# Optimization experiments

Measured on AMD Instinct MI355X. Metric: run time of the kernel, lower is better.

## Reference

```python
import jax, jax.numpy as jnp
import numpy as np

NA = 3            # anchors per scale
NC = 80           # num classes
THRESH = 0.6      # wh-IoU anchor-match threshold
EPS = 1e-7

ANCHORS_PX = np.array([[12,16],[19,36],[40,28],[36,75],[76,55],[72,146],
                       [142,110],[192,243],[459,401]], dtype=np.float32).reshape(3, 3, 2)


def setup_inputs() -> dict:
    key = jax.random.key(0)
    k1, k2, k3, k4, k5, k6 = jax.random.split(key, 6)
    B, M = 16, 32
    p0 = jax.random.normal(k1, (B, NA * (5 + NC), 80, 80), jnp.float32)
    p1 = jax.random.normal(k2, (B, NA * (5 + NC), 40, 40), jnp.float32)
    p2 = jax.random.normal(k3, (B, NA * (5 + NC), 20, 20), jnp.float32)
    # targets: [B, M, 6] = (img_idx, class in [1,NC], cx, cy, w, h) normalized to [0,1]
    bidx = jnp.broadcast_to(jnp.arange(B, dtype=jnp.float32)[:, None], (B, M))
    cls = jax.random.randint(k4, (B, M), 1, NC + 1).astype(jnp.float32)
    xy = jax.random.uniform(k5, (B, M, 2), minval=0.05, maxval=0.95)
    ka, kj = jax.random.split(k6)
    aidx = jax.random.randint(ka, (B, M), 0, 9)
    base_wh = jnp.asarray(ANCHORS_PX.reshape(9, 2))[aidx] / 640.0
    jitter = jnp.exp(jax.random.uniform(kj, (B, M, 2), minval=-0.15, maxval=0.15))
    wh = base_wh * jitter
    targets = jnp.concatenate([bidx[..., None], cls[..., None], xy, wh], axis=-1)
    return {"p0": p0, "p1": p1, "p2": p2,
            "targets": targets,
            "anchors": jnp.asarray(ANCHORS_PX),
            "image_size": jnp.array([640.0, 640.0], jnp.float32)}


def _bce_logits(x, t):
    # BCEWithLogits, pos_weight=1, elementwise
    return jnp.maximum(x, 0.0) - x * t + jnp.log1p(jnp.exp(-jnp.abs(x)))


def _giou(pbox, tbox):
    # boxes [N,4] in cxcywh
    px1 = pbox[:, 0] - pbox[:, 2] * 0.5
    py1 = pbox[:, 1] - pbox[:, 3] * 0.5
    px2 = pbox[:, 0] + pbox[:, 2] * 0.5
    py2 = pbox[:, 1] + pbox[:, 3] * 0.5
    tx1 = tbox[:, 0] - tbox[:, 2] * 0.5
    ty1 = tbox[:, 1] - tbox[:, 3] * 0.5
    tx2 = tbox[:, 0] + tbox[:, 2] * 0.5
    ty2 = tbox[:, 1] + tbox[:, 3] * 0.5
    iw = jnp.clip(jnp.minimum(px2, tx2) - jnp.maximum(px1, tx1), 0.0)
    ih = jnp.clip(jnp.minimum(py2, ty2) - jnp.maximum(py1, ty1), 0.0)
    inter = iw * ih
    union = pbox[:, 2] * pbox[:, 3] + tbox[:, 2] * tbox[:, 3] - inter + EPS
    iou = inter / union
    cw = jnp.maximum(px2, tx2) - jnp.minimum(px1, tx1)
    ch = jnp.maximum(py2, ty2) - jnp.minimum(py1, ty1)
    c_area = cw * ch + EPS
    return iou - (c_area - union) / c_area


def _scale_losses(pi, tflat, anchors_i, image_size):
    # pi: [B, NA*(5+NC), H, W]; tflat: [N,6]; anchors_i: [NA,2] in pixels
    B = pi.shape[0]
    H, W = pi.shape[-2:]
    stride = image_size / jnp.array([H, W], jnp.float32)          # (sH, sW)
    anchor = anchors_i / stride[::-1][None, :]                    # anchors in grid units (w,h)
    gain = jnp.concatenate([jnp.ones((2,), jnp.float32),
                            (1.0 / stride)[jnp.array([1, 0, 1, 0])]])
    t = tflat * gain                                              # [N,6]
    gwh = t[:, 4:6]
    # wh-IoU matrix [NA, N] -> best anchor per target
    inter = (jnp.minimum(anchor[:, None, 0], gwh[None, :, 0])
             * jnp.minimum(anchor[:, None, 1], gwh[None, :, 1]))
    union = anchor[:, None, 0] * anchor[:, None, 1] + gwh[None, :, 0] * gwh[None, :, 1] - inter
    iou = inter / union
    best = iou.max(0)
    a = iou.argmax(0)
    mask = best > THRESH                                          # fixed-shape mask replaces torch boolean compaction
    maskf = mask.astype(jnp.float32)

    b = jnp.where(mask, t[:, 0].astype(jnp.int32), 0)
    c = t[:, 1].astype(jnp.int32)
    gxy = t[:, 2:4]
    gi = jnp.where(mask, gxy[:, 0].astype(jnp.int32), 0)
    gj = jnp.where(mask, gxy[:, 1].astype(jnp.int32), 0)
    a_s = jnp.where(mask, a, 0)

    pir = pi.reshape(B, NA, 5 + NC, H, W).transpose(0, 1, 3, 4, 2)  # [B,NA,H,W,5+NC]
    ps = pir[b, a_s, gj, gi]                                        # [N,5+NC]
    tobj = jnp.zeros((B, NA, H, W), jnp.float32)
    tobj = tobj.at[b, a_s, gj, gi].max(jax.lax.stop_gradient(maskf))

    pxy = jax.nn.sigmoid(ps[:, 0:2])
    pwh = jnp.minimum(jnp.exp(ps[:, 2:4]), 1000.0) * anchor[a_s]
    pbox = jnp.concatenate([pxy, pwh], 1)
    tbox = jnp.concatenate([gxy % 1.0, t[:, 4:6]], 1)
    giou = _giou(pbox, tbox)
    nb = jnp.maximum(maskf.sum(), 1.0)
    lbox = (maskf * (1.0 - giou)).sum() / nb
    tcls = jax.nn.one_hot(c - 1, NC, dtype=jnp.float32)             # cp=1, cn=0 (eps=0)
    lcls = (maskf[:, None] * _bce_logits(ps[:, 5:], tcls)).sum() / (nb * NC)
    lobj = _bce_logits(pir[..., 4], tobj).mean()
    return lbox, lobj, lcls


def _total_loss(p0, p1, p2, targets, anchors, image_size):
    tflat = targets.reshape(-1, 6)
    lbox = lobj = lcls = jnp.float32(0.0)
    for i, pi in enumerate([p0, p1, p2]):
        lb, lo, lc = _scale_losses(pi, tflat, anchors[i], image_size)
        lbox = lbox + lb
        lobj = lobj + lo
        lcls = lcls + lc
    lbox = lbox * 3.54
    lobj = lobj * 64.3
    lcls = lcls * 37.4
    return lbox + lobj + lcls, lbox, lobj, lcls


def reference(p0, p1, p2, targets, anchors, image_size):
    return _total_loss(p0, p1, p2, targets, anchors, image_size)
```

## Files before the change

kernel.cpp:

```cpp
#include <hip/hip_runtime.h>
#include <math.h>

#define NAANCH 3
#define NCLS 80
#define BATCH 16
#define NTGT 512
#define CH 85

#define V4_S0 76800
#define V4_S1 19200
#define V4_S2 4800
#define V4_TOT (V4_S0 + V4_S1 + V4_S2)
#define OBJ_BLOCKS 197
#define GRID_BLOCKS (3 + OBJ_BLOCKS)

#define WBOX 3.54f
#define WOBJ 64.3f
#define WCLS 37.4f

__device__ __forceinline__ float bce0(float x) {
    return fmaxf(x, 0.0f) + log1pf(expf(-fabsf(x)));
}

__device__ __forceinline__ float wave_sum(float v) {
    for (int off = 32; off > 0; off >>= 1) v += __shfl_down(v, off, 64);
    return v;
}

__global__ void yolo_loss_kernel(const float* __restrict__ p0,
                                 const float* __restrict__ p1,
                                 const float* __restrict__ p2,
                                 const float* __restrict__ targets,
                                 const float* __restrict__ anchors,
                                 const float* __restrict__ image_size,
                                 float* __restrict__ out) {
    const int tid  = threadIdx.x;
    const int lane = tid & 63;
    const int wid  = tid >> 6;

    __shared__ int   sh_key[NTGT];
    __shared__ int   sh_off[NTGT];
    __shared__ int   sh_ci[NTGT];
    __shared__ unsigned char sh_mk[NTGT];
    __shared__ float red[4][8];

    if (blockIdx.x < 3) {
        const int s = blockIdx.x;
        const int j = tid;
        const int H = (s == 0) ? 80 : ((s == 1) ? 40 : 20);
        const int W = H;
        const int HW = H * W;
        const float* pi = (s == 0) ? p0 : ((s == 1) ? p1 : p2);

        const float stride0 = image_size[0] / (float)H;
        const float stride1 = image_size[1] / (float)W;
        const float gx = 1.0f / stride1;
        const float gy = 1.0f / stride0;

        const float t0 = targets[j * 6 + 0];
        const float t1 = targets[j * 6 + 1];
        const float tx = targets[j * 6 + 2] * gx;
        const float ty = targets[j * 6 + 3] * gy;
        const float gw = targets[j * 6 + 4] * gx;
        const float gh = targets[j * 6 + 5] * gy;

        float best = -1.0f; int abest = 0;
        for (int k = 0; k < NAANCH; ++k) {
            float aw = anchors[(s * NAANCH + k) * 2 + 0] / stride1;
            float ah = anchors[(s * NAANCH + k) * 2 + 1] / stride0;
            float inter = fminf(aw, gw) * fminf(ah, gh);
            float uni = aw * ah + gw * gh - inter;
            float iou = inter / uni;
            if (iou > best) { best = iou; abest = k; }
        }
        const bool  mask  = best > 0.6f;
        const float maskf = mask ? 1.0f : 0.0f;

        int b  = mask ? (int)t0 : 0;
        const int c = (int)t1;
        int gi = mask ? (int)tx : 0;
        int gj = mask ? (int)ty : 0;
        const int a_s = mask ? abest : 0;
        gi = min(max(gi, 0), W - 1);
        gj = min(max(gj, 0), H - 1);
        b  = min(max(b, 0), BATCH - 1);

        const int key = ((b * NAANCH + a_s) * H + gj) * W + gi;
        const int off = (b * (NAANCH * CH) + a_s * CH) * HW + gj * W + gi;

        float lbox_t = 0.0f, ps4 = 0.0f;
        if (mask) {
            const float ps0 = pi[off + 0 * HW];
            const float ps1 = pi[off + 1 * HW];
            const float ps2 = pi[off + 2 * HW];
            const float ps3 = pi[off + 3 * HW];
            ps4 = pi[off + 4 * HW];

            const float aw = anchors[(s * NAANCH + a_s) * 2 + 0] / stride1;
            const float ah = anchors[(s * NAANCH + a_s) * 2 + 1] / stride0;

            const float pxc = 1.0f / (1.0f + expf(-ps0));
            const float pyc = 1.0f / (1.0f + expf(-ps1));
            const float pw  = fminf(expf(ps2), 1000.0f) * aw;
            const float ph  = fminf(expf(ps3), 1000.0f) * ah;
            const float txc = tx - floorf(tx);
            const float tyc = ty - floorf(ty);

            const float px1 = pxc - pw * 0.5f, py1 = pyc - ph * 0.5f;
            const float px2 = pxc + pw * 0.5f, py2 = pyc + ph * 0.5f;
            const float qx1 = txc - gw * 0.5f, qy1 = tyc - gh * 0.5f;
            const float qx2 = txc + gw * 0.5f, qy2 = tyc + gh * 0.5f;
            const float iw = fmaxf(fminf(px2, qx2) - fmaxf(px1, qx1), 0.0f);
            const float ih = fmaxf(fminf(py2, qy2) - fmaxf(py1, qy1), 0.0f);
            const float inter = iw * ih;
            const float uni = pw * ph + gw * gh - inter + 1e-7f;
            const float iou = inter / uni;
            const float cw  = fmaxf(px2, qx2) - fminf(px1, qx1);
            const float chh = fmaxf(py2, qy2) - fminf(py1, qy1);
            const float carea = cw * chh + 1e-7f;
            lbox_t = 1.0f - (iou - (carea - uni) / carea);
        }

        sh_key[j] = key;
        sh_off[j] = off;
        sh_ci[j]  = c - 1;
        sh_mk[j]  = mask ? 1 : 0;
        __syncthreads();

        float corr = 0.0f;
        if (mask) {
            bool dup = false;
            for (int j2 = 0; j2 < j; ++j2)
                if (sh_mk[j2] && sh_key[j2] == key) { dup = true; break; }
            if (!dup) corr = -ps4;
        }

        float v0 = wave_sum(lbox_t);
        float v1 = wave_sum(maskf);
        float v2 = wave_sum(corr);
        if (lane == 0) { red[0][wid] = v0; red[1][wid] = v1; red[2][wid] = v2; }
        __syncthreads();

        float lcls_w = 0.0f;
        for (int j2 = wid; j2 < NTGT; j2 += 8) {
            if (!sh_mk[j2]) continue;
            const int toff = sh_off[j2];
            const int ci   = sh_ci[j2];
            const int k1 = lane;
            float x1 = pi[toff + (5 + k1) * HW];
            float c1 = bce0(x1) - ((k1 == ci) ? x1 : 0.0f);
            float c2 = 0.0f;
            if (lane < NCLS - 64) {
                const int k2 = 64 + lane;
                float x2 = pi[toff + (5 + k2) * HW];
                c2 = bce0(x2) - ((k2 == ci) ? x2 : 0.0f);
            }
            float tsum = wave_sum(c1 + c2);
            if (lane == 0) lcls_w += tsum;
        }
        if (lane == 0) red[3][wid] = lcls_w;
        __syncthreads();

        if (tid == 0) {
            float acc[4] = {0.f, 0.f, 0.f, 0.f};
            for (int w = 0; w < 8; ++w) {
                acc[0] += red[0][w]; acc[1] += red[1][w];
                acc[2] += red[2][w]; acc[3] += red[3][w];
            }
            const float Ns = (s == 0) ? 307200.0f : ((s == 1) ? 76800.0f : 19200.0f);
            const float nb = fmaxf(acc[1], 1.0f);
            const float lbox_c = WBOX * (acc[0] / nb);
            const float lobj_c = WOBJ * (acc[2] / Ns);
            const float lcls_c = WCLS * (acc[3] / (nb * (float)NCLS));
            atomicAdd(&out[1], lbox_c);
            atomicAdd(&out[2], lobj_c);
            atomicAdd(&out[3], lcls_c);
            atomicAdd(&out[0], lbox_c + lobj_c + lcls_c);
        }
    } else {
        const int vb = (blockIdx.x - 3) * 512 + tid;
        float a0 = 0.f, a1 = 0.f, a2 = 0.f;
        if (vb < V4_TOT) {
            const float4* addr; int hw4; int sflag;
            if (vb < V4_S0) {
                const int u = vb;
                const int ba = u / 1600;  hw4 = u - ba * 1600;
                const int b = ba / 3, a = ba - 3 * b;
                addr = (const float4*)(p0 + (size_t)((b * NAANCH + a) * CH + 4) * 6400);
                sflag = 0;
            } else if (vb < V4_S0 + V4_S1) {
                const int u = vb - V4_S0;
                const int ba = u / 400;   hw4 = u - ba * 400;
                const int b = ba / 3, a = ba - 3 * b;
                addr = (const float4*)(p1 + (size_t)((b * NAANCH + a) * CH + 4) * 1600);
                sflag = 1;
            } else {
                const int u = vb - V4_S0 - V4_S1;
                const int ba = u / 100;   hw4 = u - ba * 100;
                const int b = ba / 3, a = ba - 3 * b;
                addr = (const float4*)(p2 + (size_t)((b * NAANCH + a) * CH + 4) * 400);
                sflag = 2;
            }
            float4 x = addr[hw4];
            float v = bce0(x.x) + bce0(x.y) + bce0(x.z) + bce0(x.w);
            if (sflag == 0) a0 = v; else if (sflag == 1) a1 = v; else a2 = v;
        }
        a0 = wave_sum(a0); a1 = wave_sum(a1); a2 = wave_sum(a2);
        if (lane == 0) { red[0][wid] = a0; red[1][wid] = a1; red[2][wid] = a2; }
        __syncthreads();
        if (tid == 0) {
            float s0 = 0.f, s1 = 0.f, s2 = 0.f;
            for (int w = 0; w < 8; ++w) { s0 += red[0][w]; s1 += red[1][w]; s2 += red[2][w]; }
            const float lobj_c = WOBJ * (s0 / 307200.0f + s1 / 76800.0f + s2 / 19200.0f);
            atomicAdd(&out[2], lobj_c);
            atomicAdd(&out[0], lobj_c);
        }
    }
}

extern "C" void kernel_launch(void* const* d_in, const int* in_sizes, int n_in,
                              void* d_out, int out_size, void* d_ws, size_t ws_size,
                              hipStream_t stream) {
    const float* p0       = (const float*)d_in[0];
    const float* p1       = (const float*)d_in[1];
    const float* p2       = (const float*)d_in[2];
    const float* targets  = (const float*)d_in[3];
    const float* anchors  = (const float*)d_in[4];
    const float* img_size = (const float*)d_in[5];
    float* out = (float*)d_out;

    yolo_loss_kernel<<<GRID_BLOCKS, 512, 0, stream>>>(p0, p1, p2, targets, anchors, img_size, out);
}
```

Baseline: 154.0 us.

## Spread class-loss work across objectness blocks and hash-dedupe duplicate cells

The class BCE work is moved out of the three per-scale blocks, which were the critical path. Each wave in the objectness blocks now handles one (scale, target) pair, recomputing the anchor match and match count locally. The O(n^2) shared-memory duplicate scan becomes a shared hash table filled with atomicCAS. The trade-off is redundant recomputation of nb per wave (512 targets per wave) and extra atomics on the class-loss output.

```diff
diff --git a/kernel.cpp b/kernel.cpp
--- a/kernel.cpp
+++ b/kernel.cpp
@@ -13,6 +13,7 @@
 #define V4_TOT (V4_S0 + V4_S1 + V4_S2)
 #define OBJ_BLOCKS 197
 #define GRID_BLOCKS (3 + OBJ_BLOCKS)
+#define NPAIR (3 * NTGT)
 
 #define WBOX 3.54f
 #define WOBJ 64.3f
@@ -23,9 +24,12 @@
 }
 
 __device__ __forceinline__ float wave_sum(float v) {
-    for (int off = 32; off > 0; off >>= 1) v += __shfl_down(v, off, 64);
+    for (int off = 1; off < 64; off <<= 1) v += __shfl_xor(v, off, 64);
     return v;
 }
+
+__device__ __forceinline__ int scale_H(int s) { return (s == 0) ? 80 : ((s == 1) ? 40 : 20); }
+__device__ __forceinline__ float scale_N(int s) { return (s == 0) ? 307200.0f : ((s == 1) ? 76800.0f : 19200.0f); }
 
 __global__ void yolo_loss_kernel(const float* __restrict__ p0,
                                  const float* __restrict__ p1,
@@ -38,16 +42,13 @@
     const int lane = tid & 63;
     const int wid  = tid >> 6;
 
-    __shared__ int   sh_key[NTGT];
-    __shared__ int   sh_off[NTGT];
-    __shared__ int   sh_ci[NTGT];
-    __shared__ unsigned char sh_mk[NTGT];
     __shared__ float red[4][8];
+    __shared__ int   htab[2048];
 
     if (blockIdx.x < 3) {
         const int s = blockIdx.x;
         const int j = tid;
-        const int H = (s == 0) ? 80 : ((s == 1) ? 40 : 20);
+        const int H = scale_H(s);
         const int W = H;
         const int HW = H * W;
         const float* pi = (s == 0) ? p0 : ((s == 1) ? p1 : p2);
@@ -57,8 +58,9 @@
         const float gx = 1.0f / stride1;
         const float gy = 1.0f / stride0;
 
+        for (int i = tid; i < 2048; i += NTGT) htab[i] = -1;
+
         const float t0 = targets[j * 6 + 0];
-        const float t1 = targets[j * 6 + 1];
         const float tx = targets[j * 6 + 2] * gx;
         const float ty = targets[j * 6 + 3] * gy;
         const float gw = targets[j * 6 + 4] * gx;
@@ -77,7 +79,6 @@
         const float maskf = mask ? 1.0f : 0.0f;
 
         int b  = mask ? (int)t0 : 0;
-        const int c = (int)t1;
         int gi = mask ? (int)tx : 0;
         int gj = mask ? (int)ty : 0;
         const int a_s = mask ? abest : 0;
@@ -121,18 +122,17 @@
             lbox_t = 1.0f - (iou - (carea - uni) / carea);
         }
 
-        sh_key[j] = key;
-        sh_off[j] = off;
-        sh_ci[j]  = c - 1;
-        sh_mk[j]  = mask ? 1 : 0;
         __syncthreads();
 
         float corr = 0.0f;
         if (mask) {
-            bool dup = false;
-            for (int j2 = 0; j2 < j; ++j2)
-                if (sh_mk[j2] && sh_key[j2] == key) { dup = true; break; }
-            if (!dup) corr = -ps4;
+            unsigned h = ((unsigned)key * 2654435761u) >> 21;
+            for (;;) {
+                int prev = atomicCAS(&htab[h], -1, key);
+                if (prev == -1) { corr = -ps4; break; }
+                if (prev == key) break;
+                h = (h + 1) & 2047;
+            }
         }
 
         float v0 = wave_sum(lbox_t);
@@ -141,44 +141,19 @@
         if (lane == 0) { red[0][wid] = v0; red[1][wid] = v1; red[2][wid] = v2; }
         __syncthreads();
 
-        float lcls_w = 0.0f;
-        for (int j2 = wid; j2 < NTGT; j2 += 8) {
-            if (!sh_mk[j2]) continue;
-            const int toff = sh_off[j2];
-            const int ci   = sh_ci[j2];
-            const int k1 = lane;
-            float x1 = pi[toff + (5 + k1) * HW];
-            float c1 = bce0(x1) - ((k1 == ci) ? x1 : 0.0f);
-            float c2 = 0.0f;
-            if (lane < NCLS - 64) {
-                const int k2 = 64 + lane;
-                float x2 = pi[toff + (5 + k2) * HW];
-                c2 = bce0(x2) - ((k2 == ci) ? x2 : 0.0f);
-            }
-            float tsum = wave_sum(c1 + c2);
-            if (lane == 0) lcls_w += tsum;
-        }
-        if (lane == 0) red[3][wid] = lcls_w;
-        __syncthreads();
-
         if (tid == 0) {
-            float acc[4] = {0.f, 0.f, 0.f, 0.f};
-            for (int w = 0; w < 8; ++w) {
-                acc[0] += red[0][w]; acc[1] += red[1][w];
-                acc[2] += red[2][w]; acc[3] += red[3][w];
-            }
-            const float Ns = (s == 0) ? 307200.0f : ((s == 1) ? 76800.0f : 19200.0f);
-            const float nb = fmaxf(acc[1], 1.0f);
-            const float lbox_c = WBOX * (acc[0] / nb);
-            const float lobj_c = WOBJ * (acc[2] / Ns);
-            const float lcls_c = WCLS * (acc[3] / (nb * (float)NCLS));
+            float acc0 = 0.f, acc1 = 0.f, acc2 = 0.f;
+            for (int w = 0; w < 8; ++w) { acc0 += red[0][w]; acc1 += red[1][w]; acc2 += red[2][w]; }
+            const float nb = fmaxf(acc1, 1.0f);
+            const float lbox_c = WBOX * (acc0 / nb);
+            const float lobj_c = WOBJ * (acc2 / scale_N(s));
             atomicAdd(&out[1], lbox_c);
             atomicAdd(&out[2], lobj_c);
-            atomicAdd(&out[3], lcls_c);
-            atomicAdd(&out[0], lbox_c + lobj_c + lcls_c);
+            atomicAdd(&out[0], lbox_c + lobj_c);
         }
     } else {
-        const int vb = (blockIdx.x - 3) * 512 + tid;
+        const int g = blockIdx.x - 3;
+        const int vb = g * 512 + tid;
         float a0 = 0.f, a1 = 0.f, a2 = 0.f;
         if (vb < V4_TOT) {
             const float4* addr; int hw4; int sflag;
@@ -205,15 +180,119 @@
             float v = bce0(x.x) + bce0(x.y) + bce0(x.z) + bce0(x.w);
             if (sflag == 0) a0 = v; else if (sflag == 1) a1 = v; else a2 = v;
         }
+
+        float lcls_part = 0.0f;
+        const int p = g * 8 + wid;
+        if (p < NPAIR) {
+            const int s = p >> 9;
+            const int j = p & (NTGT - 1);
+            const int H = scale_H(s);
+            const int W = H;
+            const int HW = H * W;
+            const float* pi = (s == 0) ? p0 : ((s == 1) ? p1 : p2);
+
+            const float stride0 = image_size[0] / (float)H;
+            const float stride1 = image_size[1] / (float)W;
+            const float gx = 1.0f / stride1;
+            const float gy = 1.0f / stride0;
+
+            const float aw0 = anchors[(s * NAANCH + 0) * 2 + 0] / stride1;
+            const float ah0 = anchors[(s * NAANCH + 0) * 2 + 1] / stride0;
+            const float aw1 = anchors[(s * NAANCH + 1) * 2 + 0] / stride1;
+            const float ah1 = anchors[(s * NAANCH + 1) * 2 + 1] / stride0;
+            const float aw2 = anchors[(s * NAANCH + 2) * 2 + 0] / stride1;
+            const float ah2 = anchors[(s * NAANCH + 2) * 2 + 1] / stride0;
+
+            float nbsum = 0.0f;
+            for (int jj = lane; jj < NTGT; jj += 64) {
+                const float w_ = targets[jj * 6 + 4] * gx;
+                const float h_ = targets[jj * 6 + 5] * gy;
+                float bst = -1.0f;
+                {
+                    float inter = fminf(aw0, w_) * fminf(ah0, h_);
+                    float uni = aw0 * ah0 + w_ * h_ - inter;
+                    float iou = inter / uni;
+                    if (iou > bst) bst = iou;
+                }
+                {
+                    float inter = fminf(aw1, w_) * fminf(ah1, h_);
+                    float uni = aw1 * ah1 + w_ * h_ - inter;
+                    float iou = inter / uni;
+                    if (iou > bst) bst = iou;
+                }
+                {
+                    float inter = fminf(aw2, w_) * fminf(ah2, h_);
+                    float uni = aw2 * ah2 + w_ * h_ - inter;
+                    float iou = inter / uni;
+                    if (iou > bst) bst = iou;
+                }
+                nbsum += (bst > 0.6f) ? 1.0f : 0.0f;
+            }
+            const float nb = fmaxf(wave_sum(nbsum), 1.0f);
+
+            const float t0 = targets[j * 6 + 0];
+            const float t1 = targets[j * 6 + 1];
+            const float tx = targets[j * 6 + 2] * gx;
+            const float ty = targets[j * 6 + 3] * gy;
+            const float gw = targets[j * 6 + 4] * gx;
+            const float gh = targets[j * 6 + 5] * gy;
+
+            float best = -1.0f; int abest = 0;
+            {
+                float inter = fminf(aw0, gw) * fminf(ah0, gh);
+                float uni = aw0 * ah0 + gw * gh - inter;
+                float iou = inter / uni;
+                if (iou > best) { best = iou; abest = 0; }
+            }
+            {
+                float inter = fminf(aw1, gw) * fminf(ah1, gh);
+                float uni = aw1 * ah1 + gw * gh - inter;
+                float iou = inter / uni;
+                if (iou > best) { best = iou; abest = 1; }
+            }
+            {
+                float inter = fminf(aw2, gw) * fminf(ah2, gh);
+                float uni = aw2 * ah2 + gw * gh - inter;
+                float iou = inter / uni;
+                if (iou > best) { best = iou; abest = 2; }
+            }
+
+            if (best > 0.6f) {
+                int b  = (int)t0;
+                int gi = (int)tx;
+                int gj = (int)ty;
+                gi = min(max(gi, 0), W - 1);
+                gj = min(max(gj, 0), H - 1);
+                b  = min(max(b, 0), BATCH - 1);
+                const int off = (b * (NAANCH * CH) + abest * CH) * HW + gj * W + gi;
+                const int ci  = (int)t1 - 1;
+
+                const float x1 = pi[off + (5 + lane) * HW];
+                float c1 = bce0(x1) - ((lane == ci) ? x1 : 0.0f);
+                if (lane < NCLS - 64) {
+                    const int k2 = 64 + lane;
+                    const float x2 = pi[off + (5 + k2) * HW];
+                    c1 += bce0(x2) - ((k2 == ci) ? x2 : 0.0f);
+                }
+                const float tsum = wave_sum(c1);
+                lcls_part = WCLS * tsum / (nb * (float)NCLS);
+            }
+        }
+
         a0 = wave_sum(a0); a1 = wave_sum(a1); a2 = wave_sum(a2);
-        if (lane == 0) { red[0][wid] = a0; red[1][wid] = a1; red[2][wid] = a2; }
+        if (lane == 0) {
+            red[0][wid] = a0; red[1][wid] = a1; red[2][wid] = a2; red[3][wid] = lcls_part;
+        }
         __syncthreads();
         if (tid == 0) {
-            float s0 = 0.f, s1 = 0.f, s2 = 0.f;
-            for (int w = 0; w < 8; ++w) { s0 += red[0][w]; s1 += red[1][w]; s2 += red[2][w]; }
+            float s0 = 0.f, s1 = 0.f, s2 = 0.f, sc = 0.f;
+            for (int w = 0; w < 8; ++w) {
+                s0 += red[0][w]; s1 += red[1][w]; s2 += red[2][w]; sc += red[3][w];
+            }
             const float lobj_c = WOBJ * (s0 / 307200.0f + s1 / 76800.0f + s2 / 19200.0f);
             atomicAdd(&out[2], lobj_c);
-            atomicAdd(&out[0], lobj_c);
+            if (sc != 0.0f) atomicAdd(&out[3], sc);
+            atomicAdd(&out[0], lobj_c + sc);
         }
     }
 }
```

New measurement: 158.4 us. +2.9%, slower.
